# Kernel tuning notes

Measured on AMD Instinct MI355X. Metric: run time of the kernel, lower is better.

Reference implementation:

```python
import jax, jax.numpy as jnp
import numpy as np

N_HEADS = 16
HEAD_DIM = 64
LN_EPS = 1e-5


def setup_inputs() -> dict:
    key = jax.random.key(0)
    k1, k2, k3 = jax.random.split(key, 3)
    b, n, d = 4, 2048, 1024
    inner = N_HEADS * HEAD_DIM  # 1024
    x = jax.random.normal(k1, (b, n, d), dtype=jnp.float32)
    ln_gamma = jnp.ones((d,), dtype=jnp.float32)
    ln_beta = jnp.zeros((d,), dtype=jnp.float32)
    # torch Linear weights are [out_features, in_features]
    W_qkv = jax.random.normal(k2, (3 * inner, d), dtype=jnp.float32) * (d ** -0.5)
    W_out = jax.random.normal(k3, (d, inner), dtype=jnp.float32) * (inner ** -0.5)
    return {"x": x, "ln_gamma": ln_gamma, "ln_beta": ln_beta,
            "W_qkv": W_qkv, "W_out": W_out}


def reference(x, ln_gamma, ln_beta, W_qkv, W_out):
    b, n, d = x.shape
    scale = HEAD_DIM ** -0.5
    # LayerNorm over last dim
    mu = jnp.mean(x, axis=-1, keepdims=True)
    var = jnp.mean(jnp.square(x - mu), axis=-1, keepdims=True)
    xn = (x - mu) * jax.lax.rsqrt(var + LN_EPS) * ln_gamma + ln_beta
    # QKV projection (Linear, no bias): y = x @ W^T
    qkv = jnp.einsum('bnd,ed->bne', xn, W_qkv)  # [b, n, 3*inner]
    qkv = qkv.reshape(b, n, 3, N_HEADS, HEAD_DIM)
    q, k, v = (jnp.transpose(qkv[:, :, i], (0, 2, 1, 3)) for i in range(3))  # [b,h,n,hd]
    scores = jnp.einsum('bhqd,bhkd->bhqk', q, k) * scale  # [b,h,n,n]
    attn = jax.nn.softmax(scores, axis=-1)
    out = jnp.einsum('bhqk,bhkd->bhqd', attn, v)  # [b,h,n,hd]
    out = jnp.transpose(out, (0, 2, 1, 3)).reshape(b, n, N_HEADS * HEAD_DIM)
    return jnp.einsum('bni,di->bnd', out, W_out)
```

## Files before the change

kernel.cpp:

```cpp
#include <hip/hip_runtime.h>


typedef _Float16 h16;
typedef __attribute__((ext_vector_type(8))) _Float16 h16x8;
typedef __attribute__((ext_vector_type(4))) _Float16 h16x4;
typedef __attribute__((ext_vector_type(4))) float f32x4;

#define B_ 4
#define S_ 2048
#define D_ 1024

static __device__ __forceinline__ void async16(void* lds, const void* g) {
  __builtin_amdgcn_global_load_lds((const __attribute__((address_space(1))) void*)g,
                                   (__attribute__((address_space(3))) void*)lds,
                                   16, 0, 0);
}

static __device__ __forceinline__ float ex2(float x) {
  float r;
  asm("v_exp_f32 %0, %1" : "=v"(r) : "v"(x));
  return r;
}

__global__ __launch_bounds__(256) void ln_k(const float* __restrict__ x,
                                            const float* __restrict__ g,
                                            const float* __restrict__ be,
                                            h16* __restrict__ xn) {
  const int row = blockIdx.x;
  const int tid = threadIdx.x;
  const float4 v = ((const float4*)(x + (size_t)row * D_))[tid];
  float s = v.x + v.y + v.z + v.w;
  float s2 = v.x * v.x + v.y * v.y + v.z * v.z + v.w * v.w;
#pragma unroll
  for (int msk = 1; msk < 64; msk <<= 1) {
    s += __shfl_xor(s, msk);
    s2 += __shfl_xor(s2, msk);
  }
  __shared__ float red[8];
  const int wv = tid >> 6, ln = tid & 63;
  if (ln == 0) { red[wv] = s; red[wv + 4] = s2; }
  __syncthreads();
  s = red[0] + red[1] + red[2] + red[3];
  s2 = red[4] + red[5] + red[6] + red[7];
  const float mu = s * (1.f / D_);
  const float rs = rsqrtf(s2 * (1.f / D_) - mu * mu + 1e-5f);
  const float4 gv = ((const float4*)g)[tid];
  const float4 bv = ((const float4*)be)[tid];
  h16x4 o;
  o[0] = (h16)((v.x - mu) * rs * gv.x + bv.x);
  o[1] = (h16)((v.y - mu) * rs * gv.y + bv.y);
  o[2] = (h16)((v.z - mu) * rs * gv.z + bv.z);
  o[3] = (h16)((v.w - mu) * rs * gv.w + bv.w);
  *(h16x4*)(xn + (size_t)row * D_ + tid * 4) = o;
}

__global__ __launch_bounds__(256) void cvt_k(const float* __restrict__ in,
                                             h16* __restrict__ o, int n4) {
  const int i = blockIdx.x * 256 + threadIdx.x;
  if (i >= n4) return;
  const float4 v = ((const float4*)in)[i];
  h16x4 r;
  r[0] = (h16)v.x; r[1] = (h16)v.y; r[2] = (h16)v.z; r[3] = (h16)v.w;
  *(h16x4*)(o + (size_t)i * 4) = r;
}

__global__ __launch_bounds__(256) void vt_k(const h16* __restrict__ qkv,
                                            h16* __restrict__ vT) {
  __shared__ h16 T[64 * 72];
  const int tid = threadIdx.x;
  const int kv0 = blockIdx.x * 64;
  const int bh = blockIdx.y;
  const int b = bh >> 4, h = bh & 15;
#pragma unroll
  for (int it = 0; it < 2; ++it) {
    const int s = tid + it * 256;
    const int kv = s >> 3, sl = s & 7;
    const int wsl = sl ^ ((kv >> 3) & 7);
    const h16x8 v = *(const h16x8*)(qkv + (size_t)(b * S_ + kv0 + kv) * 3072 + 2048 + h * 64 + sl * 8);
    *(h16x8*)(T + kv * 72 + wsl * 8) = v;
  }
  __syncthreads();
#pragma unroll
  for (int it = 0; it < 2; ++it) {
    const int s = tid + it * 256;
    const int d = s >> 3, sl = s & 7;
    h16x8 v;
#pragma unroll
    for (int j = 0; j < 8; ++j) {
      const int kv = sl * 8 + j;
      v[j] = T[kv * 72 + (((d >> 3) ^ sl) & 7) * 8 + (d & 7)];
    }
    *(h16x8*)(vT + (size_t)(bh * 64 + d) * 2048 + kv0 + sl * 8) = v;
  }
}

__global__ __launch_bounds__(256, 2) void gemm2(const h16* __restrict__ A, int lda,
                                                const h16* __restrict__ Bm,
                                                float* __restrict__ Cf,
                                                h16* __restrict__ Ch,
                                                int M, int N, int K,
                                                int scale_cols, float scale) {
  __shared__ __align__(16) h16 As[2][128 * 64];
  __shared__ __align__(16) h16 Bs[2][128 * 64];
  const int tid = threadIdx.x;
  const int wv = tid >> 6, ln = tid & 63;
  const int l15 = ln & 15, l4 = ln >> 4;
  const int row0 = blockIdx.x * 128, col0 = blockIdx.y * 128;
  const int wm = (wv >> 1) * 64, wn = (wv & 1) * 64;
  f32x4 acc[4][4] = {};

  const int srow = wv * 8 + (ln >> 3);
  const int sslot = (ln & 7) ^ ((ln >> 3) & 7);
  const h16* ag = A + (size_t)(row0 + srow) * lda + sslot * 8;
  const h16* bg = Bm + (size_t)(col0 + srow) * K + sslot * 8;

#define STAGE(BUF, T) do {                                                   \
    const size_t k_ = (size_t)(T) * 64;                                      \
    async16((char*)As[BUF] + wv * 1024,          ag + k_);                   \
    async16((char*)As[BUF] + 4096 + wv * 1024,   ag + (size_t)32 * lda + k_);\
    async16((char*)As[BUF] + 8192 + wv * 1024,   ag + (size_t)64 * lda + k_);\
    async16((char*)As[BUF] + 12288 + wv * 1024,  ag + (size_t)96 * lda + k_);\
    async16((char*)Bs[BUF] + wv * 1024,          bg + k_);                   \
    async16((char*)Bs[BUF] + 4096 + wv * 1024,   bg + (size_t)32 * K + k_);  \
    async16((char*)Bs[BUF] + 8192 + wv * 1024,   bg + (size_t)64 * K + k_);  \
    async16((char*)Bs[BUF] + 12288 + wv * 1024,  bg + (size_t)96 * K + k_);  \
  } while (0)

#define GCOMPUTE(BC) do {                                                    \
    const h16* Ab_ = As[BC];                                                 \
    const h16* Bb_ = Bs[BC];                                                 \
    _Pragma("unroll")                                                        \
    for (int ks = 0; ks < 2; ++ks) {                                         \
      h16x8 af[4], bf[4];                                                    \
      _Pragma("unroll")                                                      \
      for (int i = 0; i < 4; ++i)                                            \
        af[i] = *(const h16x8*)(Ab_ + (wm + i * 16 + l15) * 64 +             \
                                (((ks * 4 + l4) ^ (l15 & 7)) * 8));          \
      _Pragma("unroll")                                                      \
      for (int j = 0; j < 4; ++j)                                            \
        bf[j] = *(const h16x8*)(Bb_ + (wn + j * 16 + l15) * 64 +             \
                                (((ks * 4 + l4) ^ (l15 & 7)) * 8));          \
      __builtin_amdgcn_s_setprio(1);                                         \
      _Pragma("unroll")                                                      \
      for (int i = 0; i < 4; ++i)                                            \
        _Pragma("unroll")                                                    \
        for (int j = 0; j < 4; ++j)                                          \
          acc[i][j] = __builtin_amdgcn_mfma_f32_16x16x32_f16(af[i], bf[j], acc[i][j], 0, 0, 0); \
      __builtin_amdgcn_s_setprio(0);                                         \
    }                                                                        \
  } while (0)

#define GBODY(T) do {                                                        \
    asm volatile("s_waitcnt lgkmcnt(0)" ::: "memory");                       \
    asm volatile("s_waitcnt vmcnt(0)" ::: "memory");                         \
    __builtin_amdgcn_sched_barrier(0);                                       \
    __builtin_amdgcn_s_barrier();                                            \
    __builtin_amdgcn_sched_barrier(0);                                       \
    if ((T) + 1 < 16) STAGE(((T) + 1) & 1, (T) + 1);                         \
    GCOMPUTE((T) & 1);                                                       \
  } while (0)

  STAGE(0, 0);
  for (int t2 = 0; t2 < 16; t2 += 2) {
    GBODY(t2 + 0);
    GBODY(t2 + 1);
  }

#pragma unroll
  for (int i = 0; i < 4; ++i)
#pragma unroll
    for (int j = 0; j < 4; ++j) {
      const int col = col0 + wn + j * 16 + l15;
      const float sc = (col < scale_cols) ? scale : 1.f;
#pragma unroll
      for (int r = 0; r < 4; ++r) {
        const int row = row0 + wm + i * 16 + l4 * 4 + r;
        const float vv = acc[i][j][r] * sc;
        if (Ch) Ch[(size_t)row * N + col] = (h16)vv;
        else    Cf[(size_t)row * N + col] = vv;
      }
    }
#undef STAGE
#undef GCOMPUTE
#undef GBODY
}

__global__ __launch_bounds__(512) void attn_k(h16* __restrict__ qkv,
                                              const h16* __restrict__ vT) {
  __shared__ __align__(16) h16 Ks[3][64 * 64];
  __shared__ __align__(16) h16 Vs[3][64 * 64];
  const int tid = threadIdx.x;
  const int wv = tid >> 6, ln = tid & 63;
  const int l15 = ln & 15, l4 = ln >> 4;
  const int bh = blockIdx.x;
  const int b = bh >> 4, h = bh & 15;
  const size_t rb = (size_t)b * S_;
  const int qb = blockIdx.y * 256 + wv * 32;

  h16x8 qf[2][2];
#pragma unroll
  for (int qb2 = 0; qb2 < 2; ++qb2)
#pragma unroll
    for (int ks = 0; ks < 2; ++ks)
      qf[qb2][ks] = *(const h16x8*)(qkv + (rb + qb + qb2 * 16 + l15) * 3072 + h * 64 + ks * 32 + l4 * 8);

  f32x4 o[2][4] = {};
  f32x4 lsum[2] = {};
  h16x8 ones8;
#pragma unroll
  for (int j = 0; j < 8; ++j) ones8[j] = (h16)1.f;

  const int srow = wv * 8 + (ln >> 3);
  const int ssl = (ln & 7) ^ (srow & 7);
  const h16* kgb = qkv + (rb + srow) * 3072 + 1024 + h * 64 + ssl * 8;

  const int vd = tid >> 3;
  const int s8 = tid & 7;
  const int vks = s8 >> 2, vb0b = s8 & 1, vhi = (s8 >> 1) & 1;
  const int vd7 = vd & 7;
  const h16* vgb = vT + (size_t)(bh * 64 + vd) * 2048 + s8 * 8;
  const int dstA = vd * 64 + (((vks * 4 + (vb0b * 2)) ^ vd7) * 8) + vhi * 4;
  const int dstB = vd * 64 + (((vks * 4 + (vb0b * 2 + 1)) ^ vd7) * 8) + vhi * 4;

  int jro[4], slx[2];
#pragma unroll
  for (int j = 0; j < 4; ++j) jro[j] = (j * 16 + l15) * 64;
#pragma unroll
  for (int ks = 0; ks < 2; ++ks) slx[ks] = ((ks * 4 + l4) ^ (l15 & 7)) * 8;

  h16x8 va, vb;

#define ISSUEK(BUF, T) do {                                                  \
    async16((char*)Ks[BUF] + wv * 1024, kgb + (size_t)(T) * 64 * 3072);      \
  } while (0)

#define VSTOREM(BUF, S0) do {                                                \
    *(h16x4*)(Vs[BUF] + dstA) = __builtin_shufflevector(S0, S0, 0, 1, 2, 3); \
    *(h16x4*)(Vs[BUF] + dstB) = __builtin_shufflevector(S0, S0, 4, 5, 6, 7); \
  } while (0)

#define COMPUTE(BC) do {                                                     \
    const h16* Kb_ = Ks[BC];                                                 \
    const h16* Vb_ = Vs[BC];                                                 \
    f32x4 st[2][4] = {};                                                     \
    __builtin_amdgcn_s_setprio(1);                                           \
    _Pragma("unroll")                                                        \
    for (int ks = 0; ks < 2; ++ks) {                                         \
      h16x8 kb[4];                                                           \
      _Pragma("unroll")                                                      \
      for (int jb = 0; jb < 4; ++jb)                                         \
        kb[jb] = *(const h16x8*)(Kb_ + jro[jb] + slx[ks]);                   \
      _Pragma("unroll")                                                      \
      for (int qq = 0; qq < 2; ++qq)                                         \
        _Pragma("unroll")                                                    \
        for (int jb = 0; jb < 4; ++jb)                                       \
          st[qq][jb] = __builtin_amdgcn_mfma_f32_16x16x32_f16(kb[jb], qf[qq][ks], st[qq][jb], 0, 0, 0); \
    }                                                                        \
    __builtin_amdgcn_s_setprio(0);                                           \
    h16x8 vfr[2][4];                                                         \
    _Pragma("unroll")                                                        \
    for (int ks = 0; ks < 2; ++ks)                                           \
      _Pragma("unroll")                                                      \
      for (int jd = 0; jd < 4; ++jd)                                         \
        vfr[ks][jd] = *(const h16x8*)(Vb_ + jro[jd] + slx[ks]);              \
    _Pragma("unroll")                                                        \
    for (int qq = 0; qq < 2; ++qq) {                                         \
      h16x8 pa[2];                                                           \
      _Pragma("unroll")                                                      \
      for (int ks = 0; ks < 2; ++ks) {                                       \
        _Pragma("unroll")                                                    \
        for (int r = 0; r < 4; ++r)                                          \
          pa[ks][r] = (h16)ex2(st[qq][2 * ks][r]);                           \
        _Pragma("unroll")                                                    \
        for (int r = 0; r < 4; ++r)                                          \
          pa[ks][4 + r] = (h16)ex2(st[qq][2 * ks + 1][r]);                   \
      }                                                                      \
      __builtin_amdgcn_s_setprio(1);                                         \
      _Pragma("unroll")                                                      \
      for (int jd = 0; jd < 4; ++jd)                                         \
        o[qq][jd] = __builtin_amdgcn_mfma_f32_16x16x32_f16(pa[0], vfr[0][jd], o[qq][jd], 0, 0, 0); \
      lsum[qq] = __builtin_amdgcn_mfma_f32_16x16x32_f16(pa[0], ones8, lsum[qq], 0, 0, 0); \
      _Pragma("unroll")                                                      \
      for (int jd = 0; jd < 4; ++jd)                                         \
        o[qq][jd] = __builtin_amdgcn_mfma_f32_16x16x32_f16(pa[1], vfr[1][jd], o[qq][jd], 0, 0, 0); \
      lsum[qq] = __builtin_amdgcn_mfma_f32_16x16x32_f16(pa[1], ones8, lsum[qq], 0, 0, 0); \
      __builtin_amdgcn_s_setprio(0);                                         \
    }                                                                        \
  } while (0)

#define ENDBAR() do {                                                        \
    asm volatile("s_waitcnt lgkmcnt(0)" ::: "memory");                       \
    __builtin_amdgcn_sched_barrier(0);                                       \
    __builtin_amdgcn_s_barrier();                                            \
  } while (0)

#define BODYM(T, BC, B1, B2, VL, VS) do {                                    \
    ISSUEK(B2, (T) + 2);                                                     \
    VL = *(const h16x8*)(vgb + ((T) + 2) * 64);                              \
    VSTOREM(B1, VS);         \
    COMPUTE(BC);                                                             \
    ENDBAR();                                                                \
  } while (0)

  ISSUEK(0, 0);
  va = *(const h16x8*)(vgb);
  ISSUEK(1, 1);
  vb = *(const h16x8*)(vgb + 64);
  VSTOREM(0, va);
  ENDBAR();

  for (int t6 = 0; t6 < 30; t6 += 6) {
    BODYM(t6 + 0, 0, 1, 2, va, vb);
    BODYM(t6 + 1, 1, 2, 0, vb, va);
    BODYM(t6 + 2, 2, 0, 1, va, vb);
    BODYM(t6 + 3, 0, 1, 2, vb, va);
    BODYM(t6 + 4, 1, 2, 0, va, vb);
    BODYM(t6 + 5, 2, 0, 1, vb, va);
  }
  VSTOREM(1, vb);
  COMPUTE(0);
  ENDBAR();
  COMPUTE(1);

#pragma unroll
  for (int qb2 = 0; qb2 < 2; ++qb2) {
    f32x4 iv;
#pragma unroll
    for (int r = 0; r < 4; ++r) iv[r] = 1.f / lsum[qb2][r];
#pragma unroll
    for (int jd = 0; jd < 4; ++jd)
#pragma unroll
      for (int r = 0; r < 4; ++r) {
        const size_t row = rb + qb + qb2 * 16 + l4 * 4 + r;
        qkv[row * 3072 + h * 64 + jd * 16 + l15] = (h16)(o[qb2][jd][r] * iv[r]);
      }
  }
#undef ISSUEK
#undef VSTOREM
#undef COMPUTE
#undef ENDBAR
#undef BODYM
}

extern "C" void kernel_launch(void* const* d_in, const int* in_sizes, int n_in,
                              void* d_out, int out_size, void* d_ws, size_t ws_size,
                              hipStream_t stream) {
  const float* x  = (const float*)d_in[0];
  const float* g  = (const float*)d_in[1];
  const float* be = (const float*)d_in[2];
  const float* wq = (const float*)d_in[3];
  const float* wo = (const float*)d_in[4];
  float* out = (float*)d_out;

  char* ws = (char*)d_ws;
  h16* xn   = (h16*)ws;
  h16* wqkv = (h16*)(ws + 16777216);
  h16* wout = (h16*)(ws + 23068672);
  h16* qkv  = (h16*)(ws + 25165824);
  h16* vT   = xn;

  ln_k<<<dim3(8192), dim3(256), 0, stream>>>(x, g, be, xn);
  cvt_k<<<dim3(3072), dim3(256), 0, stream>>>(wq, wqkv, 786432);
  cvt_k<<<dim3(1024), dim3(256), 0, stream>>>(wo, wout, 262144);
  gemm2<<<dim3(64, 24), dim3(256), 0, stream>>>(xn, 1024, wqkv, (float*)nullptr, qkv,
                                                8192, 3072, 1024, 1024, 0.18033688f);
  vt_k<<<dim3(32, 64), dim3(256), 0, stream>>>(qkv, vT);
  attn_k<<<dim3(64, 8), dim3(512), 0, stream>>>(qkv, vT);
  gemm2<<<dim3(64, 8), dim3(256), 0, stream>>>(qkv, 3072, wout, out, (h16*)nullptr,
                                               8192, 1024, 1024, 0, 1.f);
}
```

Before: 189.6 us.

## Shrink attention blocks to 4 waves with double-buffered K/V pipeline

```diff
diff --git a/kernel.cpp b/kernel.cpp
--- a/kernel.cpp
+++ b/kernel.cpp
@@ -185,17 +185,17 @@
 #undef GBODY
 }
 
-__global__ __launch_bounds__(512) void attn_k(h16* __restrict__ qkv,
-                                              const h16* __restrict__ vT) {
-  __shared__ __align__(16) h16 Ks[3][64 * 64];
-  __shared__ __align__(16) h16 Vs[3][64 * 64];
+__global__ __launch_bounds__(256, 4) void attn_k(h16* __restrict__ qkv,
+                                                 const h16* __restrict__ vT) {
+  __shared__ __align__(16) h16 Ks[2][64 * 64];
+  __shared__ __align__(16) h16 Vs[2][64 * 64];
   const int tid = threadIdx.x;
   const int wv = tid >> 6, ln = tid & 63;
   const int l15 = ln & 15, l4 = ln >> 4;
   const int bh = blockIdx.x;
   const int b = bh >> 4, h = bh & 15;
   const size_t rb = (size_t)b * S_;
-  const int qb = blockIdx.y * 256 + wv * 32;
+  const int qb = blockIdx.y * 128 + wv * 32;
 
   h16x8 qf[2][2];
 #pragma unroll
@@ -210,17 +210,20 @@
 #pragma unroll
   for (int j = 0; j < 8; ++j) ones8[j] = (h16)1.f;
 
-  const int srow = wv * 8 + (ln >> 3);
+  const int srow = wv * 16 + (ln >> 3);
   const int ssl = (ln & 7) ^ (srow & 7);
   const h16* kgb = qkv + (rb + srow) * 3072 + 1024 + h * 64 + ssl * 8;
 
-  const int vd = tid >> 3;
-  const int s8 = tid & 7;
-  const int vks = s8 >> 2, vb0b = s8 & 1, vhi = (s8 >> 1) & 1;
+  const int vd = tid >> 2;
+  const int sp = (tid & 3) * 2;
   const int vd7 = vd & 7;
-  const h16* vgb = vT + (size_t)(bh * 64 + vd) * 2048 + s8 * 8;
-  const int dstA = vd * 64 + (((vks * 4 + (vb0b * 2)) ^ vd7) * 8) + vhi * 4;
-  const int dstB = vd * 64 + (((vks * 4 + (vb0b * 2 + 1)) ^ vd7) * 8) + vhi * 4;
+  const int vhi = (sp >> 1) & 1;
+  const int vq0 = (sp >> 2) * 4;
+  const h16* vgb = vT + (size_t)(bh * 64 + vd) * 2048 + sp * 8;
+  const int d0 = vd * 64 + (((vq0 + 0) ^ vd7) * 8) + vhi * 4;
+  const int d1 = vd * 64 + (((vq0 + 1) ^ vd7) * 8) + vhi * 4;
+  const int d2 = vd * 64 + (((vq0 + 2) ^ vd7) * 8) + vhi * 4;
+  const int d3 = vd * 64 + (((vq0 + 3) ^ vd7) * 8) + vhi * 4;
 
   int jro[4], slx[2];
 #pragma unroll
@@ -228,15 +231,19 @@
 #pragma unroll
   for (int ks = 0; ks < 2; ++ks) slx[ks] = ((ks * 4 + l4) ^ (l15 & 7)) * 8;
 
-  h16x8 va, vb;
+  h16x8 va0, va1, vb0, vb1;
 
 #define ISSUEK(BUF, T) do {                                                  \
-    async16((char*)Ks[BUF] + wv * 1024, kgb + (size_t)(T) * 64 * 3072);      \
-  } while (0)
-
-#define VSTOREM(BUF, S0) do {                                                \
-    *(h16x4*)(Vs[BUF] + dstA) = __builtin_shufflevector(S0, S0, 0, 1, 2, 3); \
-    *(h16x4*)(Vs[BUF] + dstB) = __builtin_shufflevector(S0, S0, 4, 5, 6, 7); \
+    const h16* kg_ = kgb + (size_t)(T) * 64 * 3072;                          \
+    async16((char*)Ks[BUF] + wv * 2048, kg_);                                \
+    async16((char*)Ks[BUF] + wv * 2048 + 1024, kg_ + (size_t)8 * 3072);      \
+  } while (0)
+
+#define VSTOREM(BUF, S0, S1) do {                                            \
+    *(h16x4*)(Vs[BUF] + d0) = __builtin_shufflevector(S0, S0, 0, 1, 2, 3);   \
+    *(h16x4*)(Vs[BUF] + d1) = __builtin_shufflevector(S0, S0, 4, 5, 6, 7);   \
+    *(h16x4*)(Vs[BUF] + d2) = __builtin_shufflevector(S1, S1, 0, 1, 2, 3);   \
+    *(h16x4*)(Vs[BUF] + d3) = __builtin_shufflevector(S1, S1, 4, 5, 6, 7);   \
   } while (0)
 
 #define COMPUTE(BC) do {                                                     \
@@ -288,38 +295,36 @@
     }                                                                        \
   } while (0)
 
-#define ENDBAR() do {                                                        \
-    asm volatile("s_waitcnt lgkmcnt(0)" ::: "memory");                       \
+#define ENDBAR(VM) do {                                                     \
+    asm volatile("s_waitcnt vmcnt(" #VM ") lgkmcnt(0)" ::: "memory");        \
     __builtin_amdgcn_sched_barrier(0);                                       \
     __builtin_amdgcn_s_barrier();                                            \
   } while (0)
 
-#define BODYM(T, BC, B1, B2, VL, VS) do {                                    \
-    ISSUEK(B2, (T) + 2);                                                     \
-    VL = *(const h16x8*)(vgb + ((T) + 2) * 64);                              \
-    VSTOREM(B1, VS);         \
-    COMPUTE(BC);                                                             \
-    ENDBAR();                                                                \
+#define BODYA(T, VM, VS0, VS1, VL0, VL1) do {                                \
+    VSTOREM(((T) + 1) & 1, VS0, VS1);                                        \
+    ISSUEK(((T) + 1) & 1, (T) + 1);                                          \
+    if ((T) + 2 < 32) {                                                      \
+      VL0 = *(const h16x8*)(vgb + ((T) + 2) * 64);                           \
+      VL1 = *(const h16x8*)(vgb + ((T) + 2) * 64 + 8);                       \
+    }                                                                        \
+    COMPUTE((T) & 1);                                                        \
+    ENDBAR(VM);                                                              \
   } while (0)
 
   ISSUEK(0, 0);
-  va = *(const h16x8*)(vgb);
-  ISSUEK(1, 1);
-  vb = *(const h16x8*)(vgb + 64);
-  VSTOREM(0, va);
-  ENDBAR();
-
-  for (int t6 = 0; t6 < 30; t6 += 6) {
-    BODYM(t6 + 0, 0, 1, 2, va, vb);
-    BODYM(t6 + 1, 1, 2, 0, vb, va);
-    BODYM(t6 + 2, 2, 0, 1, va, vb);
-    BODYM(t6 + 3, 0, 1, 2, vb, va);
-    BODYM(t6 + 4, 1, 2, 0, va, vb);
-    BODYM(t6 + 5, 2, 0, 1, vb, va);
-  }
-  VSTOREM(1, vb);
-  COMPUTE(0);
-  ENDBAR();
+  va0 = *(const h16x8*)(vgb);
+  va1 = *(const h16x8*)(vgb + 8);
+  VSTOREM(0, va0, va1);
+  vb0 = *(const h16x8*)(vgb + 64);
+  vb1 = *(const h16x8*)(vgb + 64 + 8);
+  ENDBAR(2);
+
+  for (int t = 0; t < 30; t += 2) {
+    BODYA(t + 0, 2, vb0, vb1, va0, va1);
+    BODYA(t + 1, 2, va0, va1, vb0, vb1);
+  }
+  BODYA(30, 0, vb0, vb1, va0, va1);
   COMPUTE(1);
 
 #pragma unroll
@@ -339,7 +344,7 @@
 #undef VSTOREM
 #undef COMPUTE
 #undef ENDBAR
-#undef BODYM
+#undef BODYA
 }
 
 extern "C" void kernel_launch(void* const* d_in, const int* in_sizes, int n_in,
@@ -365,7 +370,7 @@
   gemm2<<<dim3(64, 24), dim3(256), 0, stream>>>(xn, 1024, wqkv, (float*)nullptr, qkv,
                                                 8192, 3072, 1024, 1024, 0.18033688f);
   vt_k<<<dim3(32, 64), dim3(256), 0, stream>>>(qkv, vT);
-  attn_k<<<dim3(64, 8), dim3(512), 0, stream>>>(qkv, vT);
+  attn_k<<<dim3(64, 16), dim3(256), 0, stream>>>(qkv, vT);
   gemm2<<<dim3(64, 8), dim3(256), 0, stream>>>(qkv, 3072, wout, out, (h16*)nullptr,
                                                8192, 1024, 1024, 0, 1.f);
 }
```

Measured after the change: 271.0 us. +42.9%, slower.
